# Performance work log

Hardware: AMD Instinct MI355X
Metric: run time of the kernel (lower is better)

Reference implementation:

```python
import jax, jax.numpy as jnp
import numpy as np

B0, C0, H0, W0 = 32, 512, 64, 64  # x shape; L = C0 = d_model
DC = 32   # c_increase (per-direction inner dim)
NS = 16   # d_state
RK = 32   # dt_rank = ceil(512/16)


def setup_inputs() -> dict:
    key = jax.random.key(0)
    ks = jax.random.split(key, 8)
    x = jax.random.normal(ks[0], (B0, C0, H0, W0), jnp.float32)
    xc_proj_weight = jax.random.normal(ks[1], (2, RK + 2 * NS, DC), jnp.float32) * 0.05
    dtc_projs_weight = jax.random.uniform(ks[2], (2, DC, RK), jnp.float32, -RK ** -0.5, RK ** -0.5)
    # inv-softplus of dt sampled log-uniform in [1e-3, 1e-1]
    dt = jnp.exp(jax.random.uniform(ks[3], (2, DC)) * (np.log(0.1) - np.log(0.001)) + np.log(0.001))
    dtc_projs_bias = dt + jnp.log(-jnp.expm1(-dt))
    Ac_logs = jnp.log(jnp.tile(jnp.arange(1, NS + 1, dtype=jnp.float32), (2 * DC, 1)))  # [2D, N]
    Dcs = jnp.ones((2 * DC,), jnp.float32)
    w_cin = jax.random.normal(ks[4], (DC, 2), jnp.float32) * 0.5    # Conv2d(2, DC, 1) weight
    bn_gamma = jnp.ones((DC,), jnp.float32)
    bn_beta = jnp.zeros((DC,), jnp.float32)
    bn_mean = jnp.zeros((DC,), jnp.float32)
    bn_var = jnp.ones((DC,), jnp.float32)
    w_cout = jax.random.normal(ks[5], (DC,), jnp.float32) * 0.2     # Conv2d(DC, 1, 1) weight
    ln_gamma = jnp.ones((C0,), jnp.float32)
    ln_beta = jnp.zeros((C0,), jnp.float32)
    return dict(x=x, xc_proj_weight=xc_proj_weight, dtc_projs_weight=dtc_projs_weight,
                dtc_projs_bias=dtc_projs_bias, Ac_logs=Ac_logs, Dcs=Dcs, w_cin=w_cin,
                bn_gamma=bn_gamma, bn_beta=bn_beta, bn_mean=bn_mean, bn_var=bn_var,
                w_cout=w_cout, ln_gamma=ln_gamma, ln_beta=ln_beta)


def _selective_scan(u, delta, A, Bs, Cs, D, delta_bias):
    # u, delta: [B, 2D, L]; A: [2D, N]; Bs, Cs: [B, 2, N, L] (K=2 groups); D, delta_bias: [2D]
    B, KD, L = u.shape
    d_per = KD // Bs.shape[1]
    delta = jax.nn.softplus(delta + delta_bias[None, :, None])
    Bg = jnp.repeat(Bs, d_per, axis=1)  # [B, 2D, N, L] (group = d // d_per)
    Cg = jnp.repeat(Cs, d_per, axis=1)
    dA = jnp.exp(delta[:, :, None, :] * A[None, :, :, None])      # [B, 2D, N, L]
    dBu = delta[:, :, None, :] * Bg * u[:, :, None, :]            # [B, 2D, N, L]

    def step(h, inp):
        dA_l, dBu_l = inp
        h = dA_l * h + dBu_l
        return h, h

    h0 = jnp.zeros((B, KD, dA.shape[2]), u.dtype)
    _, hs = jax.lax.scan(step, h0, (jnp.moveaxis(dA, 3, 0), jnp.moveaxis(dBu, 3, 0)))  # [L, B, 2D, N]
    y = jnp.einsum('lbdn,bdnl->bdl', hs, Cg) + D[None, :, None] * u
    return y


def reference(x, xc_proj_weight, dtc_projs_weight, dtc_projs_bias, Ac_logs, Dcs,
              w_cin, bn_gamma, bn_beta, bn_mean, bn_var, w_cout, ln_gamma, ln_beta):
    B, C, H, W = x.shape
    L = C
    avg = jnp.mean(x, axis=(2, 3))          # [B, C]
    mx = jnp.max(x, axis=(2, 3))            # [B, C]
    xsc = jnp.stack([avg, mx], axis=1)       # [B, 2, C]
    # 1x1 conv (2 -> DC) over 'spatial' dim C, + BatchNorm(eval) + GELU
    h = jnp.einsum('bic,di->bdc', xsc, w_cin)  # [B, DC, L]
    h = (h - bn_mean[None, :, None]) * jax.lax.rsqrt(bn_var + 1e-5)[None, :, None]
    h = h * bn_gamma[None, :, None] + bn_beta[None, :, None]
    h = jax.nn.gelu(h, approximate=False)
    # bidirectional stacking
    xk = jnp.stack([h, jnp.flip(h, axis=-1)], axis=1)  # [B, 2, DC, L]
    dbl = jnp.einsum('bkdl,kcd->bkcl', xk, xc_proj_weight)  # [B, 2, R+2N, L]
    dts, Bs, Cs = dbl[:, :, :RK], dbl[:, :, RK:RK + NS], dbl[:, :, RK + NS:]
    dts = jnp.einsum('bkrl,kdr->bkdl', dts, dtc_projs_weight)  # [B, 2, DC, L]
    u = xk.reshape(B, 2 * DC, L)
    delta = dts.reshape(B, 2 * DC, L)
    A = -jnp.exp(Ac_logs)  # [2D, N]
    out_y = _selective_scan(u, delta, A, Bs, Cs, Dcs, dtc_projs_bias.reshape(-1))
    out_y = out_y.reshape(B, 2, DC, L)
    y = out_y[:, 0] + jnp.flip(out_y[:, 1], axis=-1)  # [B, DC, L]
    # 1x1 conv (DC -> 1, no bias) + GELU
    y = jax.nn.gelu(jnp.einsum('bdl,d->bl', y, w_cout), approximate=False)  # [B, L]
    # LayerNorm over channel dim (d_model = C)
    mu = jnp.mean(y, axis=-1, keepdims=True)
    var = jnp.var(y, axis=-1, keepdims=True)
    attn = (y - mu) * jax.lax.rsqrt(var + 1e-5) * ln_gamma[None, :] + ln_beta[None, :]
    attn = attn[:, :, None, None]  # [B, C, 1, 1]
    return x + x * attn
```

## Files before the change

kernel.cpp:

```cpp
#include <hip/hip_runtime.h>
#include <math.h>

#define B0 32
#define C0 512
#define HW 4096
#define DC 32
#define NS 16
#define RK 32
#define L  512
#define KD 64
#define LT 128
#define CH 16
#define CL 32

__device__ __forceinline__ float gelu_exact(float x) {
    return 0.5f * x * (1.0f + erff(x * 0.70710678118654752f));
}
__device__ __forceinline__ float softplus_f(float x) {
    float ax = fabsf(x);
    return fmaxf(x, 0.0f) + log1pf(expf(-ax));
}

__global__ void pool_kernel(const float* __restrict__ x,
                            float* __restrict__ avg, float* __restrict__ mx) {
    int row = blockIdx.x;
    const float4* xr = (const float4*)(x + (size_t)row * HW);
    int tid = threadIdx.x;
    float s = 0.f, m = -INFINITY;
#pragma unroll
    for (int i = 0; i < 4; ++i) {
        float4 v = xr[tid + i * 256];
        s += v.x + v.y + v.z + v.w;
        m = fmaxf(m, fmaxf(fmaxf(v.x, v.y), fmaxf(v.z, v.w)));
    }
    for (int off = 32; off > 0; off >>= 1) {
        s += __shfl_down(s, off, 64);
        m = fmaxf(m, __shfl_down(m, off, 64));
    }
    __shared__ float ss[4], sm[4];
    int wave = tid >> 6;
    if ((tid & 63) == 0) { ss[wave] = s; sm[wave] = m; }
    __syncthreads();
    if (tid == 0) {
        s = ss[0] + ss[1] + ss[2] + ss[3];
        m = fmaxf(fmaxf(sm[0], sm[1]), fmaxf(sm[2], sm[3]));
        avg[row] = s * (1.0f / HW);
        mx[row] = m;
    }
}

__global__ void projh_kernel(const float* __restrict__ avg, const float* __restrict__ mx,
                             const float* __restrict__ w_cin,
                             const float* __restrict__ bn_g, const float* __restrict__ bn_b,
                             const float* __restrict__ bn_m, const float* __restrict__ bn_v,
                             const float* __restrict__ xcw,
                             const float* __restrict__ dtw, const float* __restrict__ dtb,
                             float* __restrict__ hout,
                             float* __restrict__ delta, float* __restrict__ Bsv,
                             float* __restrict__ Csv) {
    __shared__ float sh[DC * LT];
    __shared__ float sdt[RK * LT];
    __shared__ float sW[64 * DC];
    __shared__ float sPW[DC * RK];
    int blk = blockIdx.x;
    int lt = blk & 3;
    int k = (blk >> 2) & 1;
    int b = blk >> 3;
    int l0 = lt * LT;
    int tid = threadIdx.x;
    for (int i = tid; i < DC * LT; i += 256) {
        int d = i >> 7, l = i & (LT - 1);
        int gl = l0 + l;
        float a = avg[b * C0 + gl], m = mx[b * C0 + gl];
        float v = a * w_cin[d * 2] + m * w_cin[d * 2 + 1];
        v = (v - bn_m[d]) * rsqrtf(bn_v[d] + 1e-5f);
        v = v * bn_g[d] + bn_b[d];
        v = gelu_exact(v);
        sh[i] = v;
        if (k == 0) hout[((b * DC + d) << 9) + gl] = v;
    }
    for (int i = tid; i < 64 * DC; i += 256) sW[i] = xcw[k * 64 * DC + i];
    for (int i = tid; i < DC * RK; i += 256) sPW[i] = dtw[k * DC * RK + i];
    __syncthreads();
    for (int idx = tid; idx < 64 * LT; idx += 256) {
        int c = idx >> 7, l = idx & (LT - 1);
        float acc = 0.f;
#pragma unroll
        for (int d = 0; d < DC; ++d) acc += sh[d * LT + l] * sW[c * DC + d];
        if (c < RK) sdt[c * LT + l] = acc;
        else if (c < RK + NS)
            Bsv[(size_t)((((b * 2 + k) << 9) + l0 + l)) * NS + (c - RK)] = acc;
        else
            Csv[(size_t)((((b * 2 + k) << 9) + l0 + l)) * NS + (c - RK - NS)] = acc;
    }
    __syncthreads();
    for (int idx = tid; idx < DC * LT; idx += 256) {
        int d = idx >> 7, l = idx & (LT - 1);
        float acc = dtb[k * DC + d];
#pragma unroll
        for (int r = 0; r < RK; ++r) acc += sdt[r * LT + l] * sPW[d * RK + r];
        delta[((b * KD + k * DC + d) << 9) + l0 + l] = softplus_f(acc);
    }
}

__global__ void scanA_kernel(const float* __restrict__ h, const float* __restrict__ delta,
                             const float* __restrict__ Bsv,
                             const float* __restrict__ Ac_logs,
                             float* __restrict__ Sde, float* __restrict__ hend) {
    int blk = blockIdx.x;
    int c = blk & (CH - 1);
    int k = (blk >> 4) & 1;
    int b = blk >> 5;
    int tid = threadIdx.x;
    int d = tid >> 4;
    int n = tid & 15;
    int kd = k * DC + d;
    float A = -expf(Ac_logs[kd * NS + n]);
    const float* dp = delta + ((size_t)(b * KD + kd) << 9);
    const float* up = h + ((size_t)(b * DC + d) << 9);
    const float* Bp = Bsv + (((size_t)(b * 2 + k)) << 9) * NS;
    int s0 = c * CL;
    float hs = 0.f, sde = 0.f;
#pragma unroll 4
    for (int sl = 0; sl < CL; ++sl) {
        int s = s0 + sl;
        int l = k ? (L - 1 - s) : s;
        float de = dp[l];
        float u = up[l];
        float Bv = Bp[l * NS + n];
        hs = expf(de * A) * hs + de * Bv * u;
        sde += de;
    }
    hend[((size_t)blk * DC + d) * NS + n] = hs;
    if (n == 0) Sde[blk * DC + d] = sde;
}

__global__ void scanB_kernel(const float* __restrict__ h, const float* __restrict__ delta,
                             const float* __restrict__ Bsv, const float* __restrict__ Csv,
                             const float* __restrict__ Ac_logs, const float* __restrict__ Dcs,
                             const float* __restrict__ w_cout,
                             const float* __restrict__ Sde, const float* __restrict__ hend,
                             float* __restrict__ ybl) {
    __shared__ float red[DC][CL + 1];
    int blk = blockIdx.x;
    int c = blk & (CH - 1);
    int k = (blk >> 4) & 1;
    int b = blk >> 5;
    int tid = threadIdx.x;
    int d = tid >> 4;
    int n = tid & 15;
    int kd = k * DC + d;
    float A = -expf(Ac_logs[kd * NS + n]);
    float w = w_cout[d];
    float Dv = Dcs[kd];
    int base = (b * 2 + k) * CH;
    float carry = 0.f;
    for (int j = 0; j < c; ++j) {
        float sde = Sde[(base + j) * DC + d];
        float he = hend[((size_t)(base + j) * DC + d) * NS + n];
        carry = expf(A * sde) * carry + he;
    }
    const float* dp = delta + ((size_t)(b * KD + kd) << 9);
    const float* up = h + ((size_t)(b * DC + d) << 9);
    const float* Bp = Bsv + (((size_t)(b * 2 + k)) << 9) * NS;
    const float* Cp = Csv + (((size_t)(b * 2 + k)) << 9) * NS;
    int s0 = c * CL;
    float hs = carry;
#pragma unroll 4
    for (int sl = 0; sl < CL; ++sl) {
        int s = s0 + sl;
        int l = k ? (L - 1 - s) : s;
        float de = dp[l];
        float u = up[l];
        float Bv = Bp[l * NS + n];
        float Cv = Cp[l * NS + n];
        hs = expf(de * A) * hs + de * Bv * u;
        float contrib = hs * Cv;
        contrib += __shfl_xor(contrib, 1, 16);
        contrib += __shfl_xor(contrib, 2, 16);
        contrib += __shfl_xor(contrib, 4, 16);
        contrib += __shfl_xor(contrib, 8, 16);
        if (n == 0) red[d][sl] = w * (contrib + Dv * u);
    }
    __syncthreads();
    if (tid < CL) {
        int sl = tid;
        float acc = 0.f;
#pragma unroll
        for (int dd = 0; dd < DC; ++dd) acc += red[dd][sl];
        int s = s0 + sl;
        int l = k ? (L - 1 - s) : s;
        atomicAdd(&ybl[b * L + l], acc);
    }
}

__global__ void epi_kernel(const float* __restrict__ ybl,
                           const float* __restrict__ ln_g, const float* __restrict__ ln_b,
                           float* __restrict__ attn) {
    int b = blockIdx.x;
    int l = threadIdx.x;
    float y = gelu_exact(ybl[b * L + l]);
    float s = y, s2 = y * y;
    for (int off = 32; off > 0; off >>= 1) {
        s += __shfl_down(s, off, 64);
        s2 += __shfl_down(s2, off, 64);
    }
    __shared__ float ss[8], ss2[8];
    __shared__ float smu, srv;
    int wave = l >> 6;
    if ((l & 63) == 0) { ss[wave] = s; ss2[wave] = s2; }
    __syncthreads();
    if (l == 0) {
        float ts = 0.f, ts2 = 0.f;
#pragma unroll
        for (int i = 0; i < 8; ++i) { ts += ss[i]; ts2 += ss2[i]; }
        float mu = ts * (1.0f / L);
        float var = ts2 * (1.0f / L) - mu * mu;
        smu = mu;
        srv = rsqrtf(var + 1e-5f);
    }
    __syncthreads();
    attn[b * C0 + l] = (y - smu) * srv * ln_g[l] + ln_b[l];
}

__global__ void gate_kernel(const float* __restrict__ x, const float* __restrict__ attn,
                            float* __restrict__ out) {
    size_t t = (size_t)blockIdx.x * 256 + threadIdx.x;
    const float4* x4 = (const float4*)x;
    float4* o4 = (float4*)out;
    float4 v = x4[t];
    int bc = (int)(t >> 10);
    float a = 1.0f + attn[bc];
    v.x *= a; v.y *= a; v.z *= a; v.w *= a;
    o4[t] = v;
}

extern "C" void kernel_launch(void* const* d_in, const int* in_sizes, int n_in,
                              void* d_out, int out_size, void* d_ws, size_t ws_size,
                              hipStream_t stream) {
    const float* x     = (const float*)d_in[0];
    const float* xcw   = (const float*)d_in[1];
    const float* dtw   = (const float*)d_in[2];
    const float* dtb   = (const float*)d_in[3];
    const float* Aclog = (const float*)d_in[4];
    const float* Dcs   = (const float*)d_in[5];
    const float* wcin  = (const float*)d_in[6];
    const float* bng   = (const float*)d_in[7];
    const float* bnb   = (const float*)d_in[8];
    const float* bnm   = (const float*)d_in[9];
    const float* bnv   = (const float*)d_in[10];
    const float* wcout = (const float*)d_in[11];
    const float* lng   = (const float*)d_in[12];
    const float* lnb   = (const float*)d_in[13];
    float* out = (float*)d_out;

    float* ws = (float*)d_ws;
    float* avg   = ws;
    float* mx    = ws + 16384;
    float* h     = ws + 32768;
    float* delta = ws + 557056;
    float* Bsv   = ws + 1605632;
    float* Csv   = ws + 2129920;
    float* Sde   = ws + 2654208;
    float* hend  = ws + 2686976;
    float* ybl   = ws + 3211264;
    float* attn  = ws + 3227648;

    pool_kernel<<<B0 * C0, 256, 0, stream>>>(x, avg, mx);
    projh_kernel<<<B0 * 2 * (L / LT), 256, 0, stream>>>(avg, mx, wcin, bng, bnb, bnm, bnv,
                                                        xcw, dtw, dtb, h, delta, Bsv, Csv);
    hipMemsetAsync(ybl, 0, (size_t)B0 * L * sizeof(float), stream);
    scanA_kernel<<<B0 * 2 * CH, 512, 0, stream>>>(h, delta, Bsv, Aclog, Sde, hend);
    scanB_kernel<<<B0 * 2 * CH, 512, 0, stream>>>(h, delta, Bsv, Csv, Aclog, Dcs, wcout,
                                                  Sde, hend, ybl);
    epi_kernel<<<B0, 512, 0, stream>>>(ybl, lng, lnb, attn);
    gate_kernel<<<(B0 * C0 * HW / 4) / 256, 256, 0, stream>>>(x, attn, out);
}
```

Before: 565.6 us.

## Fuse projection and chunked selective scan into one sequential kernel per batch-direction

Merges the projection kernel and the two-pass scan kernels into a single kernel. One 512-thread block per (batch, direction) walks the sequence in 64-step chunks, keeping h, delta, B and C in shared memory. This removes the global intermediates, the memset, the atomics and the two-pass carry propagation. The trade-off is only 64 blocks and a fully serial 512-step scan per block, so parallelism drops. The gate kernel also processes 8 float4s per thread, with fewer blocks.

```diff
diff --git a/kernel.cpp b/kernel.cpp
--- a/kernel.cpp
+++ b/kernel.cpp
@@ -9,9 +9,8 @@
 #define RK 32
 #define L  512
 #define KD 64
-#define LT 128
-#define CH 16
-#define CL 32
+#define CB 64
+#define NCH (L / CB)
 
 __device__ __forceinline__ float gelu_exact(float x) {
     return 0.5f * x * (1.0f + erff(x * 0.70710678118654752f));
@@ -21,8 +20,9 @@
     return fmaxf(x, 0.0f) + log1pf(expf(-ax));
 }
 
-__global__ void pool_kernel(const float* __restrict__ x,
-                            float* __restrict__ avg, float* __restrict__ mx) {
+__global__ __launch_bounds__(256) void pool_kernel(const float* __restrict__ x,
+                                                   float* __restrict__ avg,
+                                                   float* __restrict__ mx) {
     int row = blockIdx.x;
     const float4* xr = (const float4*)(x + (size_t)row * HW);
     int tid = threadIdx.x;
@@ -49,157 +49,111 @@
     }
 }
 
-__global__ void projh_kernel(const float* __restrict__ avg, const float* __restrict__ mx,
-                             const float* __restrict__ w_cin,
-                             const float* __restrict__ bn_g, const float* __restrict__ bn_b,
-                             const float* __restrict__ bn_m, const float* __restrict__ bn_v,
-                             const float* __restrict__ xcw,
-                             const float* __restrict__ dtw, const float* __restrict__ dtb,
-                             float* __restrict__ hout,
-                             float* __restrict__ delta, float* __restrict__ Bsv,
-                             float* __restrict__ Csv) {
-    __shared__ float sh[DC * LT];
-    __shared__ float sdt[RK * LT];
+__global__ __launch_bounds__(512) void mid_kernel(
+    const float* __restrict__ avg, const float* __restrict__ mx,
+    const float* __restrict__ w_cin,
+    const float* __restrict__ bn_g, const float* __restrict__ bn_b,
+    const float* __restrict__ bn_m, const float* __restrict__ bn_v,
+    const float* __restrict__ xcw, const float* __restrict__ dtw,
+    const float* __restrict__ dtb,
+    const float* __restrict__ Ac_logs, const float* __restrict__ Dcs,
+    const float* __restrict__ w_cout,
+    float* __restrict__ ybl2)
+{
     __shared__ float sW[64 * DC];
     __shared__ float sPW[DC * RK];
+    __shared__ float sh_c[DC * (CB + 1)];
+    __shared__ float sde[DC * (CB + 1)];
+    __shared__ float sdt[RK * CB];
+    __shared__ float sB[CB * (NS + 1)];
+    __shared__ float sC[CB * (NS + 1)];
+    __shared__ float red[DC * (CB + 1)];
+
     int blk = blockIdx.x;
-    int lt = blk & 3;
-    int k = (blk >> 2) & 1;
-    int b = blk >> 3;
-    int l0 = lt * LT;
+    int k = blk & 1;
+    int b = blk >> 1;
     int tid = threadIdx.x;
-    for (int i = tid; i < DC * LT; i += 256) {
-        int d = i >> 7, l = i & (LT - 1);
-        int gl = l0 + l;
-        float a = avg[b * C0 + gl], m = mx[b * C0 + gl];
-        float v = a * w_cin[d * 2] + m * w_cin[d * 2 + 1];
-        v = (v - bn_m[d]) * rsqrtf(bn_v[d] + 1e-5f);
-        v = v * bn_g[d] + bn_b[d];
-        v = gelu_exact(v);
-        sh[i] = v;
-        if (k == 0) hout[((b * DC + d) << 9) + gl] = v;
-    }
-    for (int i = tid; i < 64 * DC; i += 256) sW[i] = xcw[k * 64 * DC + i];
-    for (int i = tid; i < DC * RK; i += 256) sPW[i] = dtw[k * DC * RK + i];
-    __syncthreads();
-    for (int idx = tid; idx < 64 * LT; idx += 256) {
-        int c = idx >> 7, l = idx & (LT - 1);
-        float acc = 0.f;
-#pragma unroll
-        for (int d = 0; d < DC; ++d) acc += sh[d * LT + l] * sW[c * DC + d];
-        if (c < RK) sdt[c * LT + l] = acc;
-        else if (c < RK + NS)
-            Bsv[(size_t)((((b * 2 + k) << 9) + l0 + l)) * NS + (c - RK)] = acc;
-        else
-            Csv[(size_t)((((b * 2 + k) << 9) + l0 + l)) * NS + (c - RK - NS)] = acc;
-    }
-    __syncthreads();
-    for (int idx = tid; idx < DC * LT; idx += 256) {
-        int d = idx >> 7, l = idx & (LT - 1);
-        float acc = dtb[k * DC + d];
-#pragma unroll
-        for (int r = 0; r < RK; ++r) acc += sdt[r * LT + l] * sPW[d * RK + r];
-        delta[((b * KD + k * DC + d) << 9) + l0 + l] = softplus_f(acc);
-    }
-}
-
-__global__ void scanA_kernel(const float* __restrict__ h, const float* __restrict__ delta,
-                             const float* __restrict__ Bsv,
-                             const float* __restrict__ Ac_logs,
-                             float* __restrict__ Sde, float* __restrict__ hend) {
-    int blk = blockIdx.x;
-    int c = blk & (CH - 1);
-    int k = (blk >> 4) & 1;
-    int b = blk >> 5;
-    int tid = threadIdx.x;
-    int d = tid >> 4;
-    int n = tid & 15;
-    int kd = k * DC + d;
-    float A = -expf(Ac_logs[kd * NS + n]);
-    const float* dp = delta + ((size_t)(b * KD + kd) << 9);
-    const float* up = h + ((size_t)(b * DC + d) << 9);
-    const float* Bp = Bsv + (((size_t)(b * 2 + k)) << 9) * NS;
-    int s0 = c * CL;
-    float hs = 0.f, sde = 0.f;
+
+    for (int i = tid; i < 64 * DC; i += 512) sW[i]  = xcw[k * 64 * DC + i];
+    for (int i = tid; i < DC * RK; i += 512) sPW[i] = dtw[k * DC * RK + i];
+
+    int d_s = tid >> 4;
+    int n_s = tid & 15;
+    int kd  = k * DC + d_s;
+    float A  = -expf(Ac_logs[kd * NS + n_s]);
+    float w  = w_cout[d_s];
+    float Dv = Dcs[kd];
+    float hs = 0.f;
+
+    for (int c = 0; c < NCH; ++c) {
+        int l0 = k ? (L - (c + 1) * CB) : c * CB;
+        __syncthreads();
+
+        for (int i = tid; i < DC * CB; i += 512) {
+            int d = i >> 6, ll = i & (CB - 1);
+            int gl = l0 + ll;
+            float a = avg[b * C0 + gl], m = mx[b * C0 + gl];
+            float v = a * w_cin[d * 2] + m * w_cin[d * 2 + 1];
+            v = (v - bn_m[d]) * rsqrtf(bn_v[d] + 1e-5f);
+            v = v * bn_g[d] + bn_b[d];
+            sh_c[d * (CB + 1) + ll] = gelu_exact(v);
+        }
+        __syncthreads();
+
+        for (int idx = tid; idx < 64 * CB; idx += 512) {
+            int cc = idx >> 6, ll = idx & (CB - 1);
+            float acc = 0.f;
+#pragma unroll
+            for (int d = 0; d < DC; ++d) acc += sh_c[d * (CB + 1) + ll] * sW[cc * DC + d];
+            if (cc < RK) sdt[cc * CB + ll] = acc;
+            else if (cc < RK + NS) sB[ll * (NS + 1) + (cc - RK)] = acc;
+            else sC[ll * (NS + 1) + (cc - RK - NS)] = acc;
+        }
+        __syncthreads();
+
+        for (int idx = tid; idx < DC * CB; idx += 512) {
+            int d = idx >> 6, ll = idx & (CB - 1);
+            float acc = dtb[k * DC + d];
+#pragma unroll
+            for (int r = 0; r < RK; ++r) acc += sdt[r * CB + ll] * sPW[d * RK + r];
+            sde[d * (CB + 1) + ll] = softplus_f(acc);
+        }
+        __syncthreads();
+
 #pragma unroll 4
-    for (int sl = 0; sl < CL; ++sl) {
-        int s = s0 + sl;
-        int l = k ? (L - 1 - s) : s;
-        float de = dp[l];
-        float u = up[l];
-        float Bv = Bp[l * NS + n];
-        hs = expf(de * A) * hs + de * Bv * u;
-        sde += de;
-    }
-    hend[((size_t)blk * DC + d) * NS + n] = hs;
-    if (n == 0) Sde[blk * DC + d] = sde;
-}
-
-__global__ void scanB_kernel(const float* __restrict__ h, const float* __restrict__ delta,
-                             const float* __restrict__ Bsv, const float* __restrict__ Csv,
-                             const float* __restrict__ Ac_logs, const float* __restrict__ Dcs,
-                             const float* __restrict__ w_cout,
-                             const float* __restrict__ Sde, const float* __restrict__ hend,
-                             float* __restrict__ ybl) {
-    __shared__ float red[DC][CL + 1];
-    int blk = blockIdx.x;
-    int c = blk & (CH - 1);
-    int k = (blk >> 4) & 1;
-    int b = blk >> 5;
-    int tid = threadIdx.x;
-    int d = tid >> 4;
-    int n = tid & 15;
-    int kd = k * DC + d;
-    float A = -expf(Ac_logs[kd * NS + n]);
-    float w = w_cout[d];
-    float Dv = Dcs[kd];
-    int base = (b * 2 + k) * CH;
-    float carry = 0.f;
-    for (int j = 0; j < c; ++j) {
-        float sde = Sde[(base + j) * DC + d];
-        float he = hend[((size_t)(base + j) * DC + d) * NS + n];
-        carry = expf(A * sde) * carry + he;
-    }
-    const float* dp = delta + ((size_t)(b * KD + kd) << 9);
-    const float* up = h + ((size_t)(b * DC + d) << 9);
-    const float* Bp = Bsv + (((size_t)(b * 2 + k)) << 9) * NS;
-    const float* Cp = Csv + (((size_t)(b * 2 + k)) << 9) * NS;
-    int s0 = c * CL;
-    float hs = carry;
-#pragma unroll 4
-    for (int sl = 0; sl < CL; ++sl) {
-        int s = s0 + sl;
-        int l = k ? (L - 1 - s) : s;
-        float de = dp[l];
-        float u = up[l];
-        float Bv = Bp[l * NS + n];
-        float Cv = Cp[l * NS + n];
-        hs = expf(de * A) * hs + de * Bv * u;
-        float contrib = hs * Cv;
-        contrib += __shfl_xor(contrib, 1, 16);
-        contrib += __shfl_xor(contrib, 2, 16);
-        contrib += __shfl_xor(contrib, 4, 16);
-        contrib += __shfl_xor(contrib, 8, 16);
-        if (n == 0) red[d][sl] = w * (contrib + Dv * u);
-    }
-    __syncthreads();
-    if (tid < CL) {
-        int sl = tid;
-        float acc = 0.f;
-#pragma unroll
-        for (int dd = 0; dd < DC; ++dd) acc += red[dd][sl];
-        int s = s0 + sl;
-        int l = k ? (L - 1 - s) : s;
-        atomicAdd(&ybl[b * L + l], acc);
-    }
-}
-
-__global__ void epi_kernel(const float* __restrict__ ybl,
-                           const float* __restrict__ ln_g, const float* __restrict__ ln_b,
-                           float* __restrict__ attn) {
+        for (int sl = 0; sl < CB; ++sl) {
+            int ll = k ? (CB - 1 - sl) : sl;
+            float de = sde[d_s * (CB + 1) + ll];
+            float u  = sh_c[d_s * (CB + 1) + ll];
+            float Bv = sB[ll * (NS + 1) + n_s];
+            float Cv = sC[ll * (NS + 1) + n_s];
+            hs = expf(de * A) * hs + de * Bv * u;
+            float contrib = hs * Cv;
+            contrib += __shfl_xor(contrib, 1, 16);
+            contrib += __shfl_xor(contrib, 2, 16);
+            contrib += __shfl_xor(contrib, 4, 16);
+            contrib += __shfl_xor(contrib, 8, 16);
+            if (n_s == 0) red[d_s * (CB + 1) + ll] = w * (contrib + Dv * u);
+        }
+        __syncthreads();
+
+        if (tid < CB) {
+            int ll = tid;
+            float acc = 0.f;
+#pragma unroll
+            for (int dd = 0; dd < DC; ++dd) acc += red[dd * (CB + 1) + ll];
+            ybl2[(size_t)blk * L + l0 + ll] = acc;
+        }
+    }
+}
+
+__global__ __launch_bounds__(512) void epi_kernel(const float* __restrict__ ybl2,
+                                                  const float* __restrict__ ln_g,
+                                                  const float* __restrict__ ln_b,
+                                                  float* __restrict__ attn) {
     int b = blockIdx.x;
     int l = threadIdx.x;
-    float y = gelu_exact(ybl[b * L + l]);
+    float y = gelu_exact(ybl2[(size_t)(b * 2) * L + l] + ybl2[(size_t)(b * 2 + 1) * L + l]);
     float s = y, s2 = y * y;
     for (int off = 32; off > 0; off >>= 1) {
         s += __shfl_down(s, off, 64);
@@ -223,16 +177,20 @@
     attn[b * C0 + l] = (y - smu) * srv * ln_g[l] + ln_b[l];
 }
 
-__global__ void gate_kernel(const float* __restrict__ x, const float* __restrict__ attn,
-                            float* __restrict__ out) {
-    size_t t = (size_t)blockIdx.x * 256 + threadIdx.x;
+__global__ __launch_bounds__(256) void gate_kernel(const float* __restrict__ x,
+                                                   const float* __restrict__ attn,
+                                                   float* __restrict__ out) {
     const float4* x4 = (const float4*)x;
     float4* o4 = (float4*)out;
-    float4 v = x4[t];
-    int bc = (int)(t >> 10);
-    float a = 1.0f + attn[bc];
-    v.x *= a; v.y *= a; v.z *= a; v.w *= a;
-    o4[t] = v;
+    size_t base = (size_t)blockIdx.x * 2048 + threadIdx.x;
+#pragma unroll
+    for (int i = 0; i < 8; ++i) {
+        size_t t = base + (size_t)i * 256;
+        float4 v = x4[t];
+        float a = 1.0f + attn[t >> 10];
+        v.x *= a; v.y *= a; v.z *= a; v.w *= a;
+        o4[t] = v;
+    }
 }
 
 extern "C" void kernel_launch(void* const* d_in, const int* in_sizes, int n_in,
@@ -255,24 +213,14 @@
     float* out = (float*)d_out;
 
     float* ws = (float*)d_ws;
-    float* avg   = ws;
-    float* mx    = ws + 16384;
-    float* h     = ws + 32768;
-    float* delta = ws + 557056;
-    float* Bsv   = ws + 1605632;
-    float* Csv   = ws + 2129920;
-    float* Sde   = ws + 2654208;
-    float* hend  = ws + 2686976;
-    float* ybl   = ws + 3211264;
-    float* attn  = ws + 3227648;
+    float* avg  = ws;
+    float* mx   = ws + 16384;
+    float* ybl2 = ws + 32768;
+    float* attn = ws + 65536;
 
     pool_kernel<<<B0 * C0, 256, 0, stream>>>(x, avg, mx);
-    projh_kernel<<<B0 * 2 * (L / LT), 256, 0, stream>>>(avg, mx, wcin, bng, bnb, bnm, bnv,
-                                                        xcw, dtw, dtb, h, delta, Bsv, Csv);
-    hipMemsetAsync(ybl, 0, (size_t)B0 * L * sizeof(float), stream);
-    scanA_kernel<<<B0 * 2 * CH, 512, 0, stream>>>(h, delta, Bsv, Aclog, Sde, hend);
-    scanB_kernel<<<B0 * 2 * CH, 512, 0, stream>>>(h, delta, Bsv, Csv, Aclog, Dcs, wcout,
-                                                  Sde, hend, ybl);
-    epi_kernel<<<B0, 512, 0, stream>>>(ybl, lng, lnb, attn);
-    gate_kernel<<<(B0 * C0 * HW / 4) / 256, 256, 0, stream>>>(x, attn, out);
-}
+    mid_kernel<<<B0 * 2, 512, 0, stream>>>(avg, mx, wcin, bng, bnb, bnm, bnv,
+                                           xcw, dtw, dtb, Aclog, Dcs, wcout, ybl2);
+    epi_kernel<<<B0, 512, 0, stream>>>(ybl2, lng, lnb, attn);
+    gate_kernel<<<(B0 * C0 * HW / 4) / 2048, 256, 0, stream>>>(x, attn, out);
+}
```

Result: slower. 677.1 us (+19.7%).
